# Optimization experiments

Measured on AMD Instinct MI355X. Metric: run time of the kernel, lower is better.

## Reference

```python
import jax, jax.numpy as jnp
import numpy as np

LAGS = 2
SLOPE = 0.2  # LeakyReLU negative slope


def _mlp(z, W0, b0, W1, b1, W2, b2, W3, b3):
    # z: [N, E+1] -> [N, 1]; 3 hidden LeakyReLU layers + linear output (MLP2, num_layers=3)
    h = jax.nn.leaky_relu(z @ W0.T + b0, SLOPE)
    h = jax.nn.leaky_relu(h @ W1.T + b1, SLOPE)
    h = jax.nn.leaky_relu(h @ W2.T + b2, SLOPE)
    return h @ W3.T + b3


def setup_inputs() -> dict:
    key = jax.random.key(0)
    ks = jax.random.split(key, 11)
    B, T, L, E, H = 64, 1000, 8, 16, 64  # batch, lags+length, latent_size, embedding_dim, hidden_dim
    x = jax.random.normal(ks[0], (B, T, L), dtype=jnp.float32)
    embeddings = jax.random.normal(ks[1], (1, T, E), dtype=jnp.float32)
    def w(k, shape, fan_in):
        return jax.random.normal(k, shape, dtype=jnp.float32) / np.float32(np.sqrt(fan_in))
    gW0 = w(ks[2], (L, H, E + 1), E + 1)
    gb0 = jax.random.normal(ks[3], (L, H), dtype=jnp.float32) * 0.05
    gW1 = w(ks[4], (L, H, H), H)
    gb1 = jax.random.normal(ks[5], (L, H), dtype=jnp.float32) * 0.05
    gW2 = w(ks[6], (L, H, H), H)
    gb2 = jax.random.normal(ks[7], (L, H), dtype=jnp.float32) * 0.05
    gW3 = w(ks[8], (L, 1, H), H)
    gb3 = jax.random.normal(ks[9], (L, 1), dtype=jnp.float32) * 0.05
    return {"x": x, "embeddings": embeddings,
            "gW0": gW0, "gb0": gb0, "gW1": gW1, "gb1": gb1,
            "gW2": gW2, "gb2": gb2, "gW3": gW3, "gb3": gb3}


def reference(x, embeddings, gW0, gb0, gW1, gb1, gW2, gb2, gW3, gb3):
    B, T, L = x.shape
    E = embeddings.shape[-1]
    length = T - LAGS
    N = B * length
    # last element of each length-(lags+1) sliding window is x[:, LAGS:]
    x_t = x[:, LAGS:, :].reshape(N, L)  # [N, L]
    emb = jnp.broadcast_to(embeddings[:, -length:], (B, length, E)).reshape(N, E)  # [N, E]
    # per-latent inputs: [L, N, E+1] (embedding shared, last coord = x_t[:, i])
    inp = jnp.concatenate(
        [jnp.broadcast_to(emb[None], (L, N, E)), x_t.T[:, :, None]], axis=-1)

    def per_latent(params, z):
        W0, b0, W1, b1, W2, b2, W3, b3 = params
        f = lambda zz: _mlp(zz, W0, b0, W1, b1, W2, b2, W3, b3)
        # jacfwd(f)(z)[:, -1] == jvp with unit tangent on last input coordinate
        tan = jnp.zeros_like(z).at[:, -1].set(1.0)
        out, dout = jax.jvp(f, (z,), (tan,))
        return out[:, 0], dout[:, 0]

    res, J = jax.vmap(per_latent)((gW0, gb0, gW1, gb1, gW2, gb2, gW3, gb3), inp)  # [L, N] each
    residuals = res.T.reshape(B, length, L)
    log_abs_det_jacobian = jnp.sum(jnp.log(jnp.abs(J)), axis=0).reshape(B, length)
    return residuals, log_abs_det_jacobian
```

## Files before the change

### kernel.cpp

```cpp
#include <hip/hip_runtime.h>

typedef unsigned short u16;
typedef unsigned int u32;
typedef float f32x4 __attribute__((ext_vector_type(4)));
typedef __fp16 f16x2 __attribute__((ext_vector_type(2)));
typedef __fp16 half8 __attribute__((ext_vector_type(8)));
typedef unsigned int uint2v __attribute__((ext_vector_type(2)));
typedef unsigned int uint4v __attribute__((ext_vector_type(4)));

#define STRW 72
#define STRU 36
#define LENT 998
#define NSAMP 63872
#define TILE_U16 4608
#define INVS 4.8828125e-4f

#define IMG_BYTES 18432
#define WS_VEC_OFF (16 * IMG_BYTES)
#define WS_E0_OFF  (WS_VEC_OFF + 8 * 256 * 4)
#define WS_NEED    ((size_t)WS_E0_OFF + (size_t)LENT * 512 * 4)

#define LDSFENCE() asm volatile("s_waitcnt lgkmcnt(0)" ::: "memory")

static __device__ __forceinline__ void gll16(const void* g, void* l) {
    __builtin_amdgcn_global_load_lds(
        (const __attribute__((address_space(1))) void*)g,
        (__attribute__((address_space(3))) void*)l, 16, 0, 0);
}

static __device__ __forceinline__ uint2v split2s(float x, float y) {
    f16x2 h = __builtin_amdgcn_cvt_pkrtz(x, y);
    f16x2 l = __builtin_amdgcn_cvt_pkrtz((x - (float)h[0]) * 2048.f,
                                         (y - (float)h[1]) * 2048.f);
    uint2v r;
    r[0] = __builtin_bit_cast(unsigned int, h);
    r[1] = __builtin_bit_cast(unsigned int, l);
    return r;
}
static __device__ __forceinline__ void split8s(f32x4 A, f32x4 B,
                                               uint4v* hi, uint4v* lo) {
    uint2v r0 = split2s(A[0], A[1]);
    uint2v r1 = split2s(A[2], A[3]);
    uint2v r2 = split2s(B[0], B[1]);
    uint2v r3 = split2s(B[2], B[3]);
    uint4v h, l;
    h[0] = r0[0]; l[0] = r0[1];
    h[1] = r1[0]; l[1] = r1[1];
    h[2] = r2[0]; l[2] = r2[1];
    h[3] = r3[0]; l[3] = r3[1];
    *hi = h; *lo = l;
}

__global__ __launch_bounds__(256) void prep_ws(
    const float* __restrict__ gW0p, const float* __restrict__ gb0p,
    const float* __restrict__ gW1p, const float* __restrict__ gb1p,
    const float* __restrict__ gW2p, const float* __restrict__ gb2p,
    const float* __restrict__ gW3p, const float* __restrict__ embp,
    char* __restrict__ ws)
{
    const int tid = threadIdx.x;
    const int bid = blockIdx.x;
    __shared__ float se[16];

    if (bid < 16) {
        const int layer = bid >> 3, l = bid & 7;
        const float* src = (layer ? gW2p : gW1p) + (size_t)l * 4096;
        u16* img = (u16*)(ws + (size_t)bid * IMG_BYTES);
        const int srow = tid >> 2, scol = (tid & 3) * 16;
        const f32x4* g = (const f32x4*)src + tid * 4;
#pragma unroll
        for (int h = 0; h < 2; ++h) {
            uint4v hi, lo;
            split8s(g[h * 2], g[h * 2 + 1], &hi, &lo);
            const int o = srow * STRW + scol + h * 8;
            *(uint4v*)&img[o] = hi;
            *(uint4v*)&img[TILE_U16 + o] = lo;
        }
        if ((tid & 3) == 3) {
            const uint4v z = {0, 0, 0, 0};
            *(uint4v*)&img[srow * STRW + 64] = z;
            *(uint4v*)&img[TILE_U16 + srow * STRW + 64] = z;
        }
        if (layer == 0 && tid < 64) {
            float* vec = (float*)(ws + WS_VEC_OFF) + l * 256;
            const float* r = gW0p + (size_t)(l * 64 + tid) * 17;
            vec[tid]       = r[16];
            vec[64 + tid]  = gb1p[l * 64 + tid];
            vec[128 + tid] = gb2p[l * 64 + tid];
            vec[192 + tid] = gW3p[l * 64 + tid];
        }
    } else {
        const int t = bid - 16;
        if (tid < 16) se[tid] = embp[(t + 2) * 16 + tid];
        __syncthreads();
        float* eo = (float*)(ws + WS_E0_OFF) + (size_t)t * 512;
#pragma unroll
        for (int p = 0; p < 2; ++p) {
            const int idx = tid + p * 256;
            const int l = idx >> 6, row = idx & 63;
            const float* r = gW0p + (size_t)(l * 64 + row) * 17;
            float acc = gb0p[l * 64 + row];
#pragma unroll
            for (int e = 0; e < 16; ++e) acc = fmaf(r[e], se[e], acc);
            eo[idx] = acc;
        }
    }
}

__global__ __launch_bounds__(256, 4) void mlp_h2(
    const float* __restrict__ xp,  const float* __restrict__ embp,
    const float* __restrict__ gW0p, const float* __restrict__ gb0p,
    const float* __restrict__ gW1p, const float* __restrict__ gb1p,
    const float* __restrict__ gW2p, const float* __restrict__ gb2p,
    const float* __restrict__ gW3p, const float* __restrict__ gb3p,
    float* __restrict__ out, const char* __restrict__ wsr, int use_ws)
{
    __shared__ u16 sW2[2][TILE_U16];
    __shared__ unsigned int scrH[4][16 * STRU];
    __shared__ unsigned int scrD[4][16 * STRU];
    __shared__ float sVec[256];
    __shared__ float sE0[64], semb[16];

    u16* const sWa = sW2[0];
    u16* const sWb = sW2[1];
    float* const sw0c = sVec;
    float* const sb1  = sVec + 64;
    float* const sb2  = sVec + 128;
    float* const sw3  = sVec + 192;

    const int tid = threadIdx.x;
    const int wave = tid >> 6, lane = tid & 63;
    const int q = lane >> 4, s = lane & 15;
    const int t = blockIdx.x;
    const int bsmp = wave * 16 + s;
    const f32x4 zf = {0.f, 0.f, 0.f, 0.f};

    if (!use_ws && tid < 16) semb[tid] = embp[(t + 2) * 16 + tid];
    float ldAcc = 0.f;

    const int srow = tid >> 2, scol = (tid & 3) * 16;

    for (int l = 0; l < 8; ++l) {
        __syncthreads();
        if (use_ws) {
            const char* img = wsr + (size_t)l * IMG_BYTES;
#pragma unroll
            for (int c = 0; c < 4; ++c)
                gll16(img + c * 4096 + tid * 16, (char*)sW2 + c * 4096 + wave * 1024);
            if (tid < 128)
                gll16(img + 16384 + tid * 16, (char*)sW2 + 16384 + wave * 1024);
            sVec[tid] = *(const float*)(wsr + WS_VEC_OFF + (size_t)(l * 256 + tid) * 4);
            if (tid < 64)
                sE0[tid] = *(const float*)(wsr + WS_E0_OFF +
                                           ((size_t)t * 512 + l * 64 + tid) * 4);
            asm volatile("s_waitcnt vmcnt(0)" ::: "memory");
        } else {
            {
                const f32x4* g = (const f32x4*)(gW1p + (size_t)l * 4096) + tid * 4;
#pragma unroll
                for (int h = 0; h < 2; ++h) {
                    uint4v hi, lo;
                    split8s(g[h * 2], g[h * 2 + 1], &hi, &lo);
                    const int o = srow * STRW + scol + h * 8;
                    *(uint4v*)&sWa[o] = hi;
                    *(uint4v*)&sWb[o] = lo;
                }
            }
            if (tid < 64) {
                const float* r = gW0p + (size_t)(l * 64 + tid) * 17;
                float acc = gb0p[l * 64 + tid];
#pragma unroll
                for (int e = 0; e < 16; e++) acc = fmaf(r[e], semb[e], acc);
                sE0[tid]  = acc;
                sw0c[tid] = r[16];
                sb1[tid]  = gb1p[l * 64 + tid];
                sb2[tid]  = gb2p[l * 64 + tid];
                sw3[tid]  = gW3p[l * 64 + tid];
            }
        }
        __syncthreads();

        const float b3v = gb3p[l];
        const float xv = xp[(size_t)(bsmp * 1000 + t + 2) * 8 + l];

        half8 H0a[2], H0b[2], D0a[2], D0b[2];
#pragma unroll
        for (int kc = 0; kc < 2; ++kc) {
            f32x4 eA = *(const f32x4*)&sE0[kc * 32 + q * 8];
            f32x4 eB = *(const f32x4*)&sE0[kc * 32 + q * 8 + 4];
            f32x4 wA = *(const f32x4*)&sw0c[kc * 32 + q * 8];
            f32x4 wB = *(const f32x4*)&sw0c[kc * 32 + q * 8 + 4];
            float hv[8], dv[8];
#pragma unroll
            for (int i = 0; i < 8; ++i) {
                float w  = (i < 4) ? wA[i] : wB[i - 4];
                float e0 = (i < 4) ? eA[i] : eB[i - 4];
                float p  = fmaf(w, xv, e0);
                hv[i] = fmaxf(p, 0.2f * p);
                dv[i] = (p >= 0.f ? 1.f : 0.2f) * w;
            }
            uint4v Ha, Hb, Da, Db;
#pragma unroll
            for (int d2 = 0; d2 < 4; ++d2) {
                uint2v rh = split2s(hv[2 * d2], hv[2 * d2 + 1]);
                uint2v rd = split2s(dv[2 * d2], dv[2 * d2 + 1]);
                Ha[d2] = rh[0]; Hb[d2] = rh[1];
                Da[d2] = rd[0]; Db[d2] = rd[1];
            }
            H0a[kc] = __builtin_bit_cast(half8, Ha);
            H0b[kc] = __builtin_bit_cast(half8, Hb);
            D0a[kc] = __builtin_bit_cast(half8, Da);
            D0b[kc] = __builtin_bit_cast(half8, Db);
        }

        f32x4 aA[4], aX[4], tA[4], tX[4];
#pragma unroll
        for (int mb = 0; mb < 4; ++mb) { aA[mb] = zf; aX[mb] = zf; tA[mb] = zf; tX[mb] = zf; }
#pragma unroll
        for (int kc = 0; kc < 2; ++kc) {
#pragma unroll
            for (int mb = 0; mb < 4; ++mb) {
                const int wo = (mb * 16 + s) * STRW + kc * 32 + q * 8;
                half8 wa = __builtin_bit_cast(half8, *(const uint4v*)&sWa[wo]);
                half8 wb = __builtin_bit_cast(half8, *(const uint4v*)&sWb[wo]);
                aA[mb] = __builtin_amdgcn_mfma_f32_16x16x32_f16(wa, H0a[kc], aA[mb], 0, 0, 0);
                aX[mb] = __builtin_amdgcn_mfma_f32_16x16x32_f16(wa, H0b[kc], aX[mb], 0, 0, 0);
                aX[mb] = __builtin_amdgcn_mfma_f32_16x16x32_f16(wb, H0a[kc], aX[mb], 0, 0, 0);
                tA[mb] = __builtin_amdgcn_mfma_f32_16x16x32_f16(wa, D0a[kc], tA[mb], 0, 0, 0);
                tX[mb] = __builtin_amdgcn_mfma_f32_16x16x32_f16(wa, D0b[kc], tX[mb], 0, 0, 0);
                tX[mb] = __builtin_amdgcn_mfma_f32_16x16x32_f16(wb, D0a[kc], tX[mb], 0, 0, 0);
            }
        }

        uint2v hpH[4], hpL[4], dpH[4], dpL[4];
#pragma unroll
        for (int mb = 0; mb < 4; ++mb) {
            f32x4 b1v = *(const f32x4*)&sb1[mb * 16 + q * 4];
            float hv[4], dv[4];
#pragma unroll
            for (int i = 0; i < 4; ++i) {
                float p  = fmaf(aX[mb][i], INVS, aA[mb][i]) + b1v[i];
                float dt = fmaf(tX[mb][i], INVS, tA[mb][i]);
                hv[i] = fmaxf(p, 0.2f * p);
                dv[i] = (p >= 0.f ? 1.f : 0.2f) * dt;
            }
            uint2v r0 = split2s(hv[0], hv[1]);
            uint2v r1 = split2s(hv[2], hv[3]);
            uint2v r2 = split2s(dv[0], dv[1]);
            uint2v r3 = split2s(dv[2], dv[3]);
            hpH[mb][0] = r0[0]; hpL[mb][0] = r0[1];
            hpH[mb][1] = r1[0]; hpL[mb][1] = r1[1];
            dpH[mb][0] = r2[0]; dpL[mb][0] = r2[1];
            dpH[mb][1] = r3[0]; dpL[mb][1] = r3[1];
        }
        unsigned int* mH = scrH[wave];
        unsigned int* mD = scrD[wave];
        half8 H1a[2], H1b[2], D1a[2], D1b[2];
#pragma unroll
        for (int mb = 0; mb < 4; ++mb) {
            *(uint2v*)&mH[s * STRU + mb * 8 + q * 2] = hpH[mb];
            *(uint2v*)&mD[s * STRU + mb * 8 + q * 2] = dpH[mb];
        }
        LDSFENCE();
#pragma unroll
        for (int kc = 0; kc < 2; ++kc) {
            H1a[kc] = __builtin_bit_cast(half8, *(const uint4v*)&mH[s * STRU + kc * 16 + q * 4]);
            D1a[kc] = __builtin_bit_cast(half8, *(const uint4v*)&mD[s * STRU + kc * 16 + q * 4]);
        }
        LDSFENCE();
#pragma unroll
        for (int mb = 0; mb < 4; ++mb) {
            *(uint2v*)&mH[s * STRU + mb * 8 + q * 2] = hpL[mb];
            *(uint2v*)&mD[s * STRU + mb * 8 + q * 2] = dpL[mb];
        }
        LDSFENCE();
#pragma unroll
        for (int kc = 0; kc < 2; ++kc) {
            H1b[kc] = __builtin_bit_cast(half8, *(const uint4v*)&mH[s * STRU + kc * 16 + q * 4]);
            D1b[kc] = __builtin_bit_cast(half8, *(const uint4v*)&mD[s * STRU + kc * 16 + q * 4]);
        }

        __syncthreads();
        if (use_ws) {
            const char* img = wsr + (size_t)(8 + l) * IMG_BYTES;
#pragma unroll
            for (int c = 0; c < 4; ++c)
                gll16(img + c * 4096 + tid * 16, (char*)sW2 + c * 4096 + wave * 1024);
            if (tid < 128)
                gll16(img + 16384 + tid * 16, (char*)sW2 + 16384 + wave * 1024);
            asm volatile("s_waitcnt vmcnt(0)" ::: "memory");
        } else {
            const f32x4* g = (const f32x4*)(gW2p + (size_t)l * 4096) + tid * 4;
#pragma unroll
            for (int h = 0; h < 2; ++h) {
                uint4v hi, lo;
                split8s(g[h * 2], g[h * 2 + 1], &hi, &lo);
                const int o = srow * STRW + scol + h * 8;
                *(uint4v*)&sWa[o] = hi;
                *(uint4v*)&sWb[o] = lo;
            }
        }
        __syncthreads();

#pragma unroll
        for (int mb = 0; mb < 4; ++mb) { aA[mb] = zf; aX[mb] = zf; tA[mb] = zf; tX[mb] = zf; }
#pragma unroll
        for (int kc = 0; kc < 2; ++kc) {
#pragma unroll
            for (int mb = 0; mb < 4; ++mb) {
                const int wo = (mb * 16 + s) * STRW + kc * 32 + q * 8;
                half8 wa = __builtin_bit_cast(half8, *(const uint4v*)&sWa[wo]);
                half8 wb = __builtin_bit_cast(half8, *(const uint4v*)&sWb[wo]);
                aA[mb] = __builtin_amdgcn_mfma_f32_16x16x32_f16(wa, H1a[kc], aA[mb], 0, 0, 0);
                aX[mb] = __builtin_amdgcn_mfma_f32_16x16x32_f16(wa, H1b[kc], aX[mb], 0, 0, 0);
                aX[mb] = __builtin_amdgcn_mfma_f32_16x16x32_f16(wb, H1a[kc], aX[mb], 0, 0, 0);
                tA[mb] = __builtin_amdgcn_mfma_f32_16x16x32_f16(wa, D1a[kc], tA[mb], 0, 0, 0);
                tX[mb] = __builtin_amdgcn_mfma_f32_16x16x32_f16(wa, D1b[kc], tX[mb], 0, 0, 0);
                tX[mb] = __builtin_amdgcn_mfma_f32_16x16x32_f16(wb, D1a[kc], tX[mb], 0, 0, 0);
            }
        }

        float rs = 0.f, js = 0.f;
#pragma unroll
        for (int mb = 0; mb < 4; ++mb) {
            f32x4 b2v = *(const f32x4*)&sb2[mb * 16 + q * 4];
            f32x4 w3v = *(const f32x4*)&sw3[mb * 16 + q * 4];
#pragma unroll
            for (int i = 0; i < 4; ++i) {
                float p  = fmaf(aX[mb][i], INVS, aA[mb][i]) + b2v[i];
                float dt = fmaf(tX[mb][i], INVS, tA[mb][i]);
                float h = fmaxf(p, 0.2f * p);
                float d = (p >= 0.f ? 1.f : 0.2f) * dt;
                rs = fmaf(w3v[i], h, rs);
                js = fmaf(w3v[i], d, js);
            }
        }
        rs += __shfl_xor(rs, 16, 64); rs += __shfl_xor(rs, 32, 64);
        js += __shfl_xor(js, 16, 64); js += __shfl_xor(js, 32, 64);
        if (lane < 16)
            out[(size_t)(bsmp * LENT + t) * 8 + l] = rs + b3v;
        ldAcc += __logf(fabsf(js));
    }

    if (lane < 16)
        out[(size_t)NSAMP * 8 + (size_t)bsmp * LENT + t] = ldAcc;
}

extern "C" void kernel_launch(void* const* d_in, const int* in_sizes, int n_in,
                              void* d_out, int out_size, void* d_ws, size_t ws_size,
                              hipStream_t stream) {
    (void)in_sizes; (void)n_in; (void)out_size;
    const int use_ws = (d_ws != nullptr && ws_size >= WS_NEED) ? 1 : 0;
    if (use_ws) {
        prep_ws<<<dim3(16 + LENT), 256, 0, stream>>>(
            (const float*)d_in[2], (const float*)d_in[3],
            (const float*)d_in[4], (const float*)d_in[5],
            (const float*)d_in[6], (const float*)d_in[7],
            (const float*)d_in[8], (const float*)d_in[1],
            (char*)d_ws);
    }
    mlp_h2<<<dim3(LENT), 256, 0, stream>>>(
        (const float*)d_in[0], (const float*)d_in[1],
        (const float*)d_in[2], (const float*)d_in[3],
        (const float*)d_in[4], (const float*)d_in[5],
        (const float*)d_in[6], (const float*)d_in[7],
        (const float*)d_in[8], (const float*)d_in[9],
        (float*)d_out, (const char*)d_ws, use_ws);
}
```

Baseline: 140.9 us.

## Prefetch next layer weights asynchronously to overlap loads with MFMA compute

Issues global_load_lds for the next weight tile right after the previous GEMM finishes, instead of loading and waiting at the start of each stage. The W2 load now overlaps the layer-1 epilogue, and the next latent's W1, bias vectors and E0 overlap the final reduction. Bias and E0 vectors are double-buffered in LDS and also loaded via async LDS DMA. This adds extra barriers, and correctness depends on the barrier placement protecting the shared weight buffer.

```diff
diff --git a/kernel.cpp b/kernel.cpp
--- a/kernel.cpp
+++ b/kernel.cpp
@@ -21,11 +21,17 @@
 #define WS_NEED    ((size_t)WS_E0_OFF + (size_t)LENT * 512 * 4)
 
 #define LDSFENCE() asm volatile("s_waitcnt lgkmcnt(0)" ::: "memory")
+#define VMFENCE()  asm volatile("s_waitcnt vmcnt(0)" ::: "memory")
 
 static __device__ __forceinline__ void gll16(const void* g, void* l) {
     __builtin_amdgcn_global_load_lds(
         (const __attribute__((address_space(1))) void*)g,
         (__attribute__((address_space(3))) void*)l, 16, 0, 0);
+}
+static __device__ __forceinline__ void gll4(const void* g, void* l) {
+    __builtin_amdgcn_global_load_lds(
+        (const __attribute__((address_space(1))) void*)g,
+        (__attribute__((address_space(3))) void*)l, 4, 0, 0);
 }
 
 static __device__ __forceinline__ uint2v split2s(float x, float y) {
@@ -118,15 +124,12 @@
     __shared__ u16 sW2[2][TILE_U16];
     __shared__ unsigned int scrH[4][16 * STRU];
     __shared__ unsigned int scrD[4][16 * STRU];
-    __shared__ float sVec[256];
-    __shared__ float sE0[64], semb[16];
+    __shared__ float sVec[2][256];
+    __shared__ float sE0[2][64];
+    __shared__ float semb[16];
 
     u16* const sWa = sW2[0];
     u16* const sWb = sW2[1];
-    float* const sw0c = sVec;
-    float* const sb1  = sVec + 64;
-    float* const sb2  = sVec + 128;
-    float* const sw3  = sVec + 192;
 
     const int tid = threadIdx.x;
     const int wave = tid >> 6, lane = tid & 63;
@@ -140,21 +143,28 @@
 
     const int srow = tid >> 2, scol = (tid & 3) * 16;
 
+    if (use_ws) {
+        const char* img = wsr;
+#pragma unroll
+        for (int c = 0; c < 4; ++c)
+            gll16(img + c * 4096 + tid * 16, (char*)sW2 + c * 4096 + wave * 1024);
+        if (tid < 128)
+            gll16(img + 16384 + tid * 16, (char*)sW2 + 16384 + wave * 1024);
+        gll4(wsr + WS_VEC_OFF + tid * 4, (char*)sVec[0] + wave * 256);
+        if (wave == 0)
+            gll4(wsr + WS_E0_OFF + (size_t)t * 2048 + lane * 4, (char*)sE0[0]);
+    }
+
     for (int l = 0; l < 8; ++l) {
-        __syncthreads();
+        const int buf = l & 1;
+        const float xv  = xp[(size_t)(bsmp * 1000 + t + 2) * 8 + l];
+        const float b3v = gb3p[l];
+
         if (use_ws) {
-            const char* img = wsr + (size_t)l * IMG_BYTES;
-#pragma unroll
-            for (int c = 0; c < 4; ++c)
-                gll16(img + c * 4096 + tid * 16, (char*)sW2 + c * 4096 + wave * 1024);
-            if (tid < 128)
-                gll16(img + 16384 + tid * 16, (char*)sW2 + 16384 + wave * 1024);
-            sVec[tid] = *(const float*)(wsr + WS_VEC_OFF + (size_t)(l * 256 + tid) * 4);
-            if (tid < 64)
-                sE0[tid] = *(const float*)(wsr + WS_E0_OFF +
-                                           ((size_t)t * 512 + l * 64 + tid) * 4);
-            asm volatile("s_waitcnt vmcnt(0)" ::: "memory");
+            VMFENCE();
+            __syncthreads();
         } else {
+            __syncthreads();
             {
                 const f32x4* g = (const f32x4*)(gW1p + (size_t)l * 4096) + tid * 4;
 #pragma unroll
@@ -171,25 +181,25 @@
                 float acc = gb0p[l * 64 + tid];
 #pragma unroll
                 for (int e = 0; e < 16; e++) acc = fmaf(r[e], semb[e], acc);
-                sE0[tid]  = acc;
-                sw0c[tid] = r[16];
-                sb1[tid]  = gb1p[l * 64 + tid];
-                sb2[tid]  = gb2p[l * 64 + tid];
-                sw3[tid]  = gW3p[l * 64 + tid];
-            }
-        }
-        __syncthreads();
-
-        const float b3v = gb3p[l];
-        const float xv = xp[(size_t)(bsmp * 1000 + t + 2) * 8 + l];
+                sE0[buf][tid]      = acc;
+                sVec[buf][tid]     = r[16];
+                sVec[buf][64 + tid]  = gb1p[l * 64 + tid];
+                sVec[buf][128 + tid] = gb2p[l * 64 + tid];
+                sVec[buf][192 + tid] = gW3p[l * 64 + tid];
+            }
+            __syncthreads();
+        }
+
+        const float* const vb = sVec[buf];
+        const float* const e0b = sE0[buf];
 
         half8 H0a[2], H0b[2], D0a[2], D0b[2];
 #pragma unroll
         for (int kc = 0; kc < 2; ++kc) {
-            f32x4 eA = *(const f32x4*)&sE0[kc * 32 + q * 8];
-            f32x4 eB = *(const f32x4*)&sE0[kc * 32 + q * 8 + 4];
-            f32x4 wA = *(const f32x4*)&sw0c[kc * 32 + q * 8];
-            f32x4 wB = *(const f32x4*)&sw0c[kc * 32 + q * 8 + 4];
+            f32x4 eA = *(const f32x4*)&e0b[kc * 32 + q * 8];
+            f32x4 eB = *(const f32x4*)&e0b[kc * 32 + q * 8 + 4];
+            f32x4 wA = *(const f32x4*)&vb[kc * 32 + q * 8];
+            f32x4 wB = *(const f32x4*)&vb[kc * 32 + q * 8 + 4];
             float hv[8], dv[8];
 #pragma unroll
             for (int i = 0; i < 8; ++i) {
@@ -232,10 +242,20 @@
             }
         }
 
+        __syncthreads();
+        if (use_ws) {
+            const char* img = wsr + (size_t)(8 + l) * IMG_BYTES;
+#pragma unroll
+            for (int c = 0; c < 4; ++c)
+                gll16(img + c * 4096 + tid * 16, (char*)sW2 + c * 4096 + wave * 1024);
+            if (tid < 128)
+                gll16(img + 16384 + tid * 16, (char*)sW2 + 16384 + wave * 1024);
+        }
+
         uint2v hpH[4], hpL[4], dpH[4], dpL[4];
 #pragma unroll
         for (int mb = 0; mb < 4; ++mb) {
-            f32x4 b1v = *(const f32x4*)&sb1[mb * 16 + q * 4];
+            f32x4 b1v = *(const f32x4*)&vb[64 + mb * 16 + q * 4];
             float hv[4], dv[4];
 #pragma unroll
             for (int i = 0; i < 4; ++i) {
@@ -280,16 +300,7 @@
             D1b[kc] = __builtin_bit_cast(half8, *(const uint4v*)&mD[s * STRU + kc * 16 + q * 4]);
         }
 
-        __syncthreads();
-        if (use_ws) {
-            const char* img = wsr + (size_t)(8 + l) * IMG_BYTES;
-#pragma unroll
-            for (int c = 0; c < 4; ++c)
-                gll16(img + c * 4096 + tid * 16, (char*)sW2 + c * 4096 + wave * 1024);
-            if (tid < 128)
-                gll16(img + 16384 + tid * 16, (char*)sW2 + 16384 + wave * 1024);
-            asm volatile("s_waitcnt vmcnt(0)" ::: "memory");
-        } else {
+        if (!use_ws) {
             const f32x4* g = (const f32x4*)(gW2p + (size_t)l * 4096) + tid * 4;
 #pragma unroll
             for (int h = 0; h < 2; ++h) {
@@ -299,6 +310,8 @@
                 *(uint4v*)&sWa[o] = hi;
                 *(uint4v*)&sWb[o] = lo;
             }
+        } else {
+            VMFENCE();
         }
         __syncthreads();
 
@@ -320,11 +333,26 @@
             }
         }
 
+        __syncthreads();
+        if (use_ws && l < 7) {
+            const char* img = wsr + (size_t)(l + 1) * IMG_BYTES;
+#pragma unroll
+            for (int c = 0; c < 4; ++c)
+                gll16(img + c * 4096 + tid * 16, (char*)sW2 + c * 4096 + wave * 1024);
+            if (tid < 128)
+                gll16(img + 16384 + tid * 16, (char*)sW2 + 16384 + wave * 1024);
+            gll4(wsr + WS_VEC_OFF + (l + 1) * 1024 + tid * 4,
+                 (char*)sVec[buf ^ 1] + wave * 256);
+            if (wave == 0)
+                gll4(wsr + WS_E0_OFF + ((size_t)t * 512 + (l + 1) * 64) * 4 + lane * 4,
+                     (char*)sE0[buf ^ 1]);
+        }
+
         float rs = 0.f, js = 0.f;
 #pragma unroll
         for (int mb = 0; mb < 4; ++mb) {
-            f32x4 b2v = *(const f32x4*)&sb2[mb * 16 + q * 4];
-            f32x4 w3v = *(const f32x4*)&sw3[mb * 16 + q * 4];
+            f32x4 b2v = *(const f32x4*)&vb[128 + mb * 16 + q * 4];
+            f32x4 w3v = *(const f32x4*)&vb[192 + mb * 16 + q * 4];
 #pragma unroll
             for (int i = 0; i < 4; ++i) {
                 float p  = fmaf(aX[mb][i], INVS, aA[mb][i]) + b2v[i];
```

New measurement: 145.0 us. 3.0% more time.

## Feed layer-2 MFMA directly from accumulator registers via 16x16x16 layout, skip LDS transpose

Applied to the files above, without the earlier changes.

Switches the second hidden-layer matmuls to the 16x16x16 f16 MFMA so that the layer-1 accumulator layout can be used directly as the B operand. This removes the per-wave LDS scratch round trip (stores, fences, reloads) for the hidden activations and tangents. The W2 prefetch now starts before the activation epilogue so the load overlaps with that compute. The tangent path is split into a separate MFMA pass after the value pass. The trade-off is twice as many smaller MFMA instructions and smaller per-lane weight loads from LDS.

```diff
diff --git a/kernel.cpp b/kernel.cpp
--- a/kernel.cpp
+++ b/kernel.cpp
@@ -4,12 +4,12 @@
 typedef unsigned int u32;
 typedef float f32x4 __attribute__((ext_vector_type(4)));
 typedef __fp16 f16x2 __attribute__((ext_vector_type(2)));
+typedef __fp16 half4 __attribute__((ext_vector_type(4)));
 typedef __fp16 half8 __attribute__((ext_vector_type(8)));
 typedef unsigned int uint2v __attribute__((ext_vector_type(2)));
 typedef unsigned int uint4v __attribute__((ext_vector_type(4)));
 
 #define STRW 72
-#define STRU 36
 #define LENT 998
 #define NSAMP 63872
 #define TILE_U16 4608
@@ -20,7 +20,7 @@
 #define WS_E0_OFF  (WS_VEC_OFF + 8 * 256 * 4)
 #define WS_NEED    ((size_t)WS_E0_OFF + (size_t)LENT * 512 * 4)
 
-#define LDSFENCE() asm volatile("s_waitcnt lgkmcnt(0)" ::: "memory")
+#define VMFENCE()  asm volatile("s_waitcnt vmcnt(0)" ::: "memory")
 
 static __device__ __forceinline__ void gll16(const void* g, void* l) {
     __builtin_amdgcn_global_load_lds(
@@ -116,8 +116,6 @@
     float* __restrict__ out, const char* __restrict__ wsr, int use_ws)
 {
     __shared__ u16 sW2[2][TILE_U16];
-    __shared__ unsigned int scrH[4][16 * STRU];
-    __shared__ unsigned int scrD[4][16 * STRU];
     __shared__ float sVec[256];
     __shared__ float sE0[64], semb[16];
 
@@ -153,7 +151,7 @@
             if (tid < 64)
                 sE0[tid] = *(const float*)(wsr + WS_E0_OFF +
                                            ((size_t)t * 512 + l * 64 + tid) * 4);
-            asm volatile("s_waitcnt vmcnt(0)" ::: "memory");
+            VMFENCE();
         } else {
             {
                 const f32x4* g = (const f32x4*)(gW1p + (size_t)l * 4096) + tid * 4;
@@ -232,64 +230,39 @@
             }
         }
 
-        uint2v hpH[4], hpL[4], dpH[4], dpL[4];
+        __syncthreads();
+        if (use_ws) {
+            const char* img = wsr + (size_t)(8 + l) * IMG_BYTES;
+#pragma unroll
+            for (int c = 0; c < 4; ++c)
+                gll16(img + c * 4096 + tid * 16, (char*)sW2 + c * 4096 + wave * 1024);
+            if (tid < 128)
+                gll16(img + 16384 + tid * 16, (char*)sW2 + 16384 + wave * 1024);
+        }
+
+        half4 H1a[4], H1b[4];
+        float dvv[4][4];
 #pragma unroll
         for (int mb = 0; mb < 4; ++mb) {
             f32x4 b1v = *(const f32x4*)&sb1[mb * 16 + q * 4];
-            float hv[4], dv[4];
+            float hv[4];
 #pragma unroll
             for (int i = 0; i < 4; ++i) {
                 float p  = fmaf(aX[mb][i], INVS, aA[mb][i]) + b1v[i];
                 float dt = fmaf(tX[mb][i], INVS, tA[mb][i]);
                 hv[i] = fmaxf(p, 0.2f * p);
-                dv[i] = (p >= 0.f ? 1.f : 0.2f) * dt;
-            }
-            uint2v r0 = split2s(hv[0], hv[1]);
-            uint2v r1 = split2s(hv[2], hv[3]);
-            uint2v r2 = split2s(dv[0], dv[1]);
-            uint2v r3 = split2s(dv[2], dv[3]);
-            hpH[mb][0] = r0[0]; hpL[mb][0] = r0[1];
-            hpH[mb][1] = r1[0]; hpL[mb][1] = r1[1];
-            dpH[mb][0] = r2[0]; dpL[mb][0] = r2[1];
-            dpH[mb][1] = r3[0]; dpL[mb][1] = r3[1];
-        }
-        unsigned int* mH = scrH[wave];
-        unsigned int* mD = scrD[wave];
-        half8 H1a[2], H1b[2], D1a[2], D1b[2];
-#pragma unroll
-        for (int mb = 0; mb < 4; ++mb) {
-            *(uint2v*)&mH[s * STRU + mb * 8 + q * 2] = hpH[mb];
-            *(uint2v*)&mD[s * STRU + mb * 8 + q * 2] = dpH[mb];
-        }
-        LDSFENCE();
-#pragma unroll
-        for (int kc = 0; kc < 2; ++kc) {
-            H1a[kc] = __builtin_bit_cast(half8, *(const uint4v*)&mH[s * STRU + kc * 16 + q * 4]);
-            D1a[kc] = __builtin_bit_cast(half8, *(const uint4v*)&mD[s * STRU + kc * 16 + q * 4]);
-        }
-        LDSFENCE();
-#pragma unroll
-        for (int mb = 0; mb < 4; ++mb) {
-            *(uint2v*)&mH[s * STRU + mb * 8 + q * 2] = hpL[mb];
-            *(uint2v*)&mD[s * STRU + mb * 8 + q * 2] = dpL[mb];
-        }
-        LDSFENCE();
-#pragma unroll
-        for (int kc = 0; kc < 2; ++kc) {
-            H1b[kc] = __builtin_bit_cast(half8, *(const uint4v*)&mH[s * STRU + kc * 16 + q * 4]);
-            D1b[kc] = __builtin_bit_cast(half8, *(const uint4v*)&mD[s * STRU + kc * 16 + q * 4]);
-        }
-
-        __syncthreads();
-        if (use_ws) {
-            const char* img = wsr + (size_t)(8 + l) * IMG_BYTES;
-#pragma unroll
-            for (int c = 0; c < 4; ++c)
-                gll16(img + c * 4096 + tid * 16, (char*)sW2 + c * 4096 + wave * 1024);
-            if (tid < 128)
-                gll16(img + 16384 + tid * 16, (char*)sW2 + 16384 + wave * 1024);
-            asm volatile("s_waitcnt vmcnt(0)" ::: "memory");
-        } else {
+                dvv[mb][i] = (p >= 0.f ? 1.f : 0.2f) * dt;
+            }
+            uint2v rh0 = split2s(hv[0], hv[1]);
+            uint2v rh1 = split2s(hv[2], hv[3]);
+            uint2v Ha, Hb;
+            Ha[0] = rh0[0]; Ha[1] = rh1[0];
+            Hb[0] = rh0[1]; Hb[1] = rh1[1];
+            H1a[mb] = __builtin_bit_cast(half4, Ha);
+            H1b[mb] = __builtin_bit_cast(half4, Hb);
+        }
+
+        if (!use_ws) {
             const f32x4* g = (const f32x4*)(gW2p + (size_t)l * 4096) + tid * 4;
 #pragma unroll
             for (int h = 0; h < 2; ++h) {
@@ -299,42 +272,74 @@
                 *(uint4v*)&sWa[o] = hi;
                 *(uint4v*)&sWb[o] = lo;
             }
-        }
-        __syncthreads();
-
-#pragma unroll
-        for (int mb = 0; mb < 4; ++mb) { aA[mb] = zf; aX[mb] = zf; tA[mb] = zf; tX[mb] = zf; }
-#pragma unroll
-        for (int kc = 0; kc < 2; ++kc) {
+        } else {
+            VMFENCE();
+        }
+        __syncthreads();
+
+        f32x4 vA[4], vX[4];
+#pragma unroll
+        for (int mb = 0; mb < 4; ++mb) { vA[mb] = zf; vX[mb] = zf; }
+#pragma unroll
+        for (int kc = 0; kc < 4; ++kc) {
 #pragma unroll
             for (int mb = 0; mb < 4; ++mb) {
-                const int wo = (mb * 16 + s) * STRW + kc * 32 + q * 8;
-                half8 wa = __builtin_bit_cast(half8, *(const uint4v*)&sWa[wo]);
-                half8 wb = __builtin_bit_cast(half8, *(const uint4v*)&sWb[wo]);
-                aA[mb] = __builtin_amdgcn_mfma_f32_16x16x32_f16(wa, H1a[kc], aA[mb], 0, 0, 0);
-                aX[mb] = __builtin_amdgcn_mfma_f32_16x16x32_f16(wa, H1b[kc], aX[mb], 0, 0, 0);
-                aX[mb] = __builtin_amdgcn_mfma_f32_16x16x32_f16(wb, H1a[kc], aX[mb], 0, 0, 0);
-                tA[mb] = __builtin_amdgcn_mfma_f32_16x16x32_f16(wa, D1a[kc], tA[mb], 0, 0, 0);
-                tX[mb] = __builtin_amdgcn_mfma_f32_16x16x32_f16(wa, D1b[kc], tX[mb], 0, 0, 0);
-                tX[mb] = __builtin_amdgcn_mfma_f32_16x16x32_f16(wb, D1a[kc], tX[mb], 0, 0, 0);
-            }
-        }
-
-        float rs = 0.f, js = 0.f;
+                const int wo = (mb * 16 + s) * STRW + kc * 16 + q * 4;
+                half4 wa = __builtin_bit_cast(half4, *(const uint2v*)&sWa[wo]);
+                half4 wb = __builtin_bit_cast(half4, *(const uint2v*)&sWb[wo]);
+                vA[mb] = __builtin_amdgcn_mfma_f32_16x16x16f16(wa, H1a[kc], vA[mb], 0, 0, 0);
+                vX[mb] = __builtin_amdgcn_mfma_f32_16x16x16f16(wa, H1b[kc], vX[mb], 0, 0, 0);
+                vX[mb] = __builtin_amdgcn_mfma_f32_16x16x16f16(wb, H1a[kc], vX[mb], 0, 0, 0);
+            }
+        }
+        float rs = 0.f;
+        float sel2[4][4];
 #pragma unroll
         for (int mb = 0; mb < 4; ++mb) {
             f32x4 b2v = *(const f32x4*)&sb2[mb * 16 + q * 4];
             f32x4 w3v = *(const f32x4*)&sw3[mb * 16 + q * 4];
 #pragma unroll
             for (int i = 0; i < 4; ++i) {
-                float p  = fmaf(aX[mb][i], INVS, aA[mb][i]) + b2v[i];
-                float dt = fmaf(tX[mb][i], INVS, tA[mb][i]);
+                float p = fmaf(vX[mb][i], INVS, vA[mb][i]) + b2v[i];
                 float h = fmaxf(p, 0.2f * p);
-                float d = (p >= 0.f ? 1.f : 0.2f) * dt;
                 rs = fmaf(w3v[i], h, rs);
-                js = fmaf(w3v[i], d, js);
-            }
-        }
+                sel2[mb][i] = (p >= 0.f ? 1.f : 0.2f) * w3v[i];
+            }
+        }
+
+        half4 D1a[4], D1b[4];
+#pragma unroll
+        for (int mb = 0; mb < 4; ++mb) {
+            uint2v rd0 = split2s(dvv[mb][0], dvv[mb][1]);
+            uint2v rd1 = split2s(dvv[mb][2], dvv[mb][3]);
+            uint2v Da, Db;
+            Da[0] = rd0[0]; Da[1] = rd1[0];
+            Db[0] = rd0[1]; Db[1] = rd1[1];
+            D1a[mb] = __builtin_bit_cast(half4, Da);
+            D1b[mb] = __builtin_bit_cast(half4, Db);
+        }
+        f32x4 dA[4], dX[4];
+#pragma unroll
+        for (int mb = 0; mb < 4; ++mb) { dA[mb] = zf; dX[mb] = zf; }
+#pragma unroll
+        for (int kc = 0; kc < 4; ++kc) {
+#pragma unroll
+            for (int mb = 0; mb < 4; ++mb) {
+                const int wo = (mb * 16 + s) * STRW + kc * 16 + q * 4;
+                half4 wa = __builtin_bit_cast(half4, *(const uint2v*)&sWa[wo]);
+                half4 wb = __builtin_bit_cast(half4, *(const uint2v*)&sWb[wo]);
+                dA[mb] = __builtin_amdgcn_mfma_f32_16x16x16f16(wa, D1a[kc], dA[mb], 0, 0, 0);
+                dX[mb] = __builtin_amdgcn_mfma_f32_16x16x16f16(wa, D1b[kc], dX[mb], 0, 0, 0);
+                dX[mb] = __builtin_amdgcn_mfma_f32_16x16x16f16(wb, D1a[kc], dX[mb], 0, 0, 0);
+            }
+        }
+        float js = 0.f;
+#pragma unroll
+        for (int mb = 0; mb < 4; ++mb)
+#pragma unroll
+            for (int i = 0; i < 4; ++i)
+                js = fmaf(sel2[mb][i], fmaf(dX[mb][i], INVS, dA[mb][i]), js);
+
         rs += __shfl_xor(rs, 16, 64); rs += __shfl_xor(rs, 32, 64);
         js += __shfl_xor(js, 16, 64); js += __shfl_xor(js, 32, 64);
         if (lane < 16)
```

After: 182.9 us. +29.8%, slower.
